# Optimization experiments

Hardware: AMD Instinct MI355X
Metric: run time of the kernel (lower is better)

The kernel has to match this reference:

```python
import jax, jax.numpy as jnp
import numpy as np

MU = 23.359
STD = 1.41
Q_LIM = 500.0
DAY = 24.0 * 3600.0
WEEK = 7.0 * DAY


def setup_inputs() -> dict:
    key = jax.random.key(0)
    ks = jax.random.split(key, 6)
    n, n_rooms, h, T, n_tout = 256, 254, 64, 50000, 2048
    m = 1 + n_rooms  # u = [Tout, Q_per_room]
    t_eval = jnp.arange(T, dtype=jnp.float32) * 30.0
    # Hurwitz A: slow RC thermal dynamics (eigenvalues ~ -1e-4 1/s)
    A = 1e-4 * (0.3 * jax.random.normal(ks[0], (n, n), jnp.float32) / np.sqrt(n)
                - jnp.eye(n, dtype=jnp.float32))
    B = 1e-6 * jax.random.uniform(ks[1], (n, m), jnp.float32)
    cooling = jax.random.uniform(ks[2], (n_rooms, 1), jnp.float32)
    w1 = 0.05 * jax.random.normal(ks[3], (h, n + 4), jnp.float32)
    b1 = jnp.zeros((h,), jnp.float32)
    w2 = 0.1 * jax.random.normal(ks[4], (h,), jnp.float32)
    # outside-temperature interpolation table covering [0, T*30+30]
    tout_ts = jnp.linspace(0.0, float(T) * 30.0 + 30.0, n_tout, dtype=jnp.float32)
    tout_vals = 10.0 + 5.0 * jax.random.normal(ks[5], (n_tout,), jnp.float32)
    return dict(t_eval=t_eval, A=A, B=B, cooling=cooling, w1=w1, b1=b1, w2=w2,
                tout_ts=tout_ts, tout_vals=tout_vals)


def _integrate(t_eval, A, B, cooling, w1, b1, w2, tout_ts, tout_vals):
    n = A.shape[0]
    # transform=sigmoid then heat_scaling(Q_lim)
    heat = jax.nn.sigmoid(cooling[:, 0]) * Q_LIM  # [n_rooms]
    t0 = t_eval[0]
    ts = t_eval - t0
    dt = ts[1] - ts[0]
    iv = 26.0 * jnp.ones((n,), jnp.float32)

    def action_of(x, t):
        xn = (x - MU) / STD
        sig = jnp.stack([jnp.sin(t * (2.0 * jnp.pi / DAY)),
                         jnp.cos(t * (2.0 * jnp.pi / DAY)),
                         jnp.sin(t * (2.0 * jnp.pi / WEEK)),
                         jnp.cos(t * (2.0 * jnp.pi / WEEK))])
        s = jnp.concatenate([xn, sig])  # [n+4]
        return jax.nn.sigmoid(jnp.dot(w2, jnp.tanh(w1 @ s + b1)))  # scalar action

    def f(x, t, Q):
        # dy/dt = A x + B u,  u = [Tout(t+t0), Q]
        Tout = jnp.interp(t + t0, tout_ts, tout_vals)
        u = jnp.concatenate([Tout[None], Q])
        return A @ x + B @ u

    def step(x, t):
        # policy action held over the RK4 substeps (30 s policy hold == dt)
        Q = -heat * action_of(x, t)
        k1 = f(x, t, Q)
        k2 = f(x + 0.5 * dt * k1, t + 0.5 * dt, Q)
        k3 = f(x + 0.5 * dt * k2, t + 0.5 * dt, Q)
        k4 = f(x + dt * k3, t + dt, Q)
        x_new = x + (dt / 6.0) * (k1 + 2.0 * k2 + 2.0 * k3 + k4)
        return x_new, x  # emit state AT t (odeint returns iv first)

    _, traj = jax.lax.scan(step, iv, ts)
    return traj  # [T, n]


_integrate_jit = jax.jit(_integrate)


def reference(t_eval, A, B, cooling, w1, b1, w2, tout_ts, tout_vals):
    return _integrate_jit(t_eval, A, B, cooling, w1, b1, w2, tout_ts, tout_vals)
```

## Files before the change

### kernel.cpp

```cpp
#include <hip/hip_runtime.h>
#include <math.h>

#define NN 256
#define HH 64

typedef unsigned int uint32;
typedef _Float16 h2f __attribute__((ext_vector_type(2)));

__device__ __forceinline__ float sigm(float x) { return 1.0f / (1.0f + expf(-x)); }

__device__ __forceinline__ float dot2(uint32 a, uint32 b, float c) {
#if __has_builtin(__builtin_amdgcn_fdot2)
    return __builtin_amdgcn_fdot2(__builtin_bit_cast(h2f, a),
                                  __builtin_bit_cast(h2f, b), c, false);
#else
    h2f x = __builtin_bit_cast(h2f, a), y = __builtin_bit_cast(h2f, b);
    return c + (float)x[0] * (float)y[0] + (float)x[1] * (float)y[1];
#endif
}

__global__ void k_affine(const float* __restrict__ A, float* __restrict__ Pout,
                         const float* __restrict__ tev, int div)
{
    int i = blockIdx.x, j = threadIdx.x;
    double h = (double)tev[1] - (double)tev[0];
    double v = (i == j ? 1.0 : 0.0) + (h / (double)div) * (double)A[i * NN + j];
    Pout[i * NN + j] = (float)v;
}

__global__ void k_gemm(const float* __restrict__ A, const float* __restrict__ Pin,
                       float* __restrict__ Pout, const float* __restrict__ tev, int div)
{
    int i = blockIdx.x, j = threadIdx.x;
    double h = (double)tev[1] - (double)tev[0];
    const float* Ar = A + i * NN;
    double acc = 0.0;
    for (int k = 0; k < NN; ++k) acc += (double)Ar[k] * (double)Pin[k * NN + j];
    double v = (i == j ? 1.0 : 0.0) + (h / (double)div) * acc;
    Pout[i * NN + j] = (float)v;
}

__global__ void k_prep_vec(const float* __restrict__ A, const float* __restrict__ B,
                           const float* __restrict__ cooling, const float* __restrict__ tev,
                           const float* __restrict__ R, float* __restrict__ gq)
{
    __shared__ float heat[NN];
    __shared__ float vin[NN];
    int t = threadIdx.x;
    double h = (double)tev[1] - (double)tev[0];
    heat[t] = (t < NN - 2) ? 500.0f * sigm(cooling[t]) : 0.0f;
    __syncthreads();
    float B0 = B[t * (NN - 1)];
    double bh = 0.0;
    for (int j = 0; j < NN - 2; ++j) bh += (double)B[t * (NN - 1) + 1 + j] * (double)heat[j];
    vin[t] = B0; __syncthreads();
    double v1 = 0.0; for (int k = 0; k < NN; ++k) v1 += (double)A[t * NN + k] * (double)vin[k];
    __syncthreads(); vin[t] = (float)v1; __syncthreads();
    double v2 = 0.0; for (int k = 0; k < NN; ++k) v2 += (double)A[t * NN + k] * (double)vin[k];
    __syncthreads(); vin[t] = (float)v2; __syncthreads();
    double v3 = 0.0; for (int k = 0; k < NN; ++k) v3 += (double)A[t * NN + k] * (double)vin[k];
    __syncthreads();
    vin[t] = (float)bh; __syncthreads();
    double u1 = 0.0; for (int k = 0; k < NN; ++k) u1 += (double)A[t * NN + k] * (double)vin[k];
    __syncthreads(); vin[t] = (float)u1; __syncthreads();
    double u2 = 0.0; for (int k = 0; k < NN; ++k) u2 += (double)A[t * NN + k] * (double)vin[k];
    __syncthreads(); vin[t] = (float)u2; __syncthreads();
    double u3 = 0.0; for (int k = 0; k < NN; ++k) u3 += (double)A[t * NN + k] * (double)vin[k];

    double srow = 0.0;
    for (int c = 0; c < NN; ++c) srow += (double)R[t * NN + c];
    srow -= 1.0;

    gq[t]        = (float)((h / 6.0) * (double)B0);
    gq[256 + t]  = (float)((h * h / 6.0) * v1);
    gq[512 + t]  = (float)((h * h * h / 12.0) * v2);
    gq[768 + t]  = (float)((h * h * h * h / 24.0) * v3);
    gq[1024 + t] = (float)(h * bh + (h * h / 2.0) * u1 + (h * h * h / 6.0) * u2
                           + (h * h * h * h / 24.0) * u3);
    gq[1280 + t] = (float)(23.359 * srow);
}

__device__ __forceinline__ float interp1(float x, const float* __restrict__ ts,
                                         const float* __restrict__ vs, int n)
{
    int lo = 0, hi = n;
    while (lo < hi) { int mid = (lo + hi) >> 1; if (ts[mid] <= x) lo = mid + 1; else hi = mid; }
    int i = lo; if (i < 1) i = 1; if (i > n - 1) i = n - 1;
    float xim = ts[i - 1], xi = ts[i];
    float fim = vs[i - 1], fi = vs[i];
    return fim + (x - xim) / (xi - xim) * (fi - fim);
}

__global__ void k_time(const float* __restrict__ tev, const float* __restrict__ tts,
                       const float* __restrict__ tvals, float* __restrict__ td,
                       int T, int ntout)
{
    int k = blockIdx.x * blockDim.x + threadIdx.x;
    if (k >= T) return;
    float t0 = tev[0];
    float dtf = tev[1] - t0;
    float t = tev[k] - t0;
    const float cD = (float)(2.0 * M_PI / 86400.0);
    const float cW = (float)(2.0 * M_PI / 604800.0);
    float f0 = (float)sin((double)(t * cD));
    float f1 = (float)cos((double)(t * cD));
    float f2 = (float)sin((double)(t * cW));
    float f3 = (float)cos((double)(t * cW));
    float To1 = interp1(t + t0, tts, tvals, ntout);
    float To2 = interp1((t + 0.5f * dtf) + t0, tts, tvals, ntout);
    float To4 = interp1((t + dtf) + t0, tts, tvals, ntout);
    size_t o = (size_t)k * 8;
    td[o + 0] = To1 + 4.0f * To2 + To4;
    td[o + 1] = To1 + 2.0f * To2;
    td[o + 2] = To1 + To2;
    td[o + 3] = To1;
    td[o + 4] = f0; td[o + 5] = f1; td[o + 6] = f2; td[o + 7] = f3;
}

__global__ void k_packE(const float* __restrict__ R, uint32* __restrict__ Epk)
{
    int d = blockIdx.x * 256 + threadIdx.x;
    int t = d >> 6, i = d & 63;
    int r = t & 255, hf = t >> 8;
    int c = hf * 128 + 2 * i;
    float e0 = 64.0f * (R[r * NN + c]     - (r == c     ? 1.0f : 0.0f));
    float e1 = 64.0f * (R[r * NN + c + 1] - (r == c + 1 ? 1.0f : 0.0f));
    union { _Float16 h[2]; uint32 u; } p;
    p.h[0] = (_Float16)e0; p.h[1] = (_Float16)e1;
    Epk[d] = p.u;
}

__global__ void k_packW(const float* __restrict__ w1, uint32* __restrict__ w1pk)
{
    int d = blockIdx.x * 256 + threadIdx.x;
    int t = d >> 4, sd = d & 15;
    int jr = t >> 3, c = t & 7;
    int j = sd >> 1, p = sd & 1;
    int col = c * 4 + j * 32 + 2 * p;
    const float is = 1.0f / 1.41f;
    union { _Float16 h[2]; uint32 u; } q;
    q.h[0] = (_Float16)(w1[jr * 260 + col] * is);
    q.h[1] = (_Float16)(w1[jr * 260 + col + 1] * is);
    w1pk[d] = q.u;
}

__global__ __launch_bounds__(512, 2) void k_main(
    const float* __restrict__ tdata, const uint32* Epk,
    const uint32* __restrict__ w1pk, const float* __restrict__ gq,
    const float* __restrict__ w1g, const float* __restrict__ b1g,
    const float* __restrict__ w2g, float* out, int T)
{
    __shared__ __align__(16) uint32 spk[132];
    __shared__ __align__(16) float xbuf[NN];
    __shared__ __align__(16) float part[2][NN];
    __shared__ float gql[6 * NN];
    __shared__ float wf[6 * HH];
    __shared__ float hid[HH];
    __shared__ float b1eff[HH];
    __shared__ float td[2][8];

    const int t = threadIdx.x;
    const int r = t & 255;
    const int hf = t >> 8;
    const int jr = t >> 3;
    const int c2 = (t & 7) * 2;
    const int lane = t & 63;

    uint32 Ereg[64];
    {
        const uint4* Eg = reinterpret_cast<const uint4*>(Epk) + (size_t)t * 16;
        #pragma unroll
        for (int i = 0; i < 16; ++i) {
            uint4 v = Eg[i];
            Ereg[4 * i + 0] = v.x; Ereg[4 * i + 1] = v.y;
            Ereg[4 * i + 2] = v.z; Ereg[4 * i + 3] = v.w;
        }
    }
    uint32 w1reg[16];
    {
        const uint4* Wg = reinterpret_cast<const uint4*>(w1pk) + (size_t)t * 4;
        #pragma unroll
        for (int i = 0; i < 4; ++i) {
            uint4 v = Wg[i];
            w1reg[4 * i + 0] = v.x; w1reg[4 * i + 1] = v.y;
            w1reg[4 * i + 2] = v.z; w1reg[4 * i + 3] = v.w;
        }
    }
    for (int i = t; i < 6 * NN; i += 512) gql[i] = gq[i];
    if (t < HH) {
        wf[t]       = w1g[t * 260 + 256];
        wf[64 + t]  = w1g[t * 260 + 257];
        wf[128 + t] = w1g[t * 260 + 258];
        wf[192 + t] = w1g[t * 260 + 259];
        wf[256 + t] = b1g[t];
        wf[320 + t] = w2g[t];
    }
    _Float16* sph = reinterpret_cast<_Float16*>(spk);
    if (t < NN) {
        xbuf[t] = 26.0f;
        sph[t] = (_Float16)(26.0f - 23.359f);
    }
    if (t < 8) td[0][t] = tdata[t];
    __syncthreads();
    if (t < HH)
        b1eff[t] = wf[256 + t] + wf[t] * td[0][4] + wf[64 + t] * td[0][5]
                 + wf[128 + t] * td[0][6] + wf[192 + t] * td[0][7];
    __syncthreads();

    const uint4* sp4 = reinterpret_cast<const uint4*>(spk);

    for (int k = 0; k < T; ++k) {
        const int cur = k & 1, nxt = cur ^ 1;
        float tdp = 0.0f;
        if (t >= 504 && k + 1 < T) tdp = tdata[(size_t)(k + 1) * 8 + (t - 504)];

        float hs = 0.0f;
        {
            #pragma unroll
            for (int j = 0; j < 8; ++j) {
                uint2 sx = *reinterpret_cast<const uint2*>(spk + c2 + j * 16);
                hs = dot2(w1reg[2 * j], sx.x, hs);
                hs = dot2(w1reg[2 * j + 1], sx.y, hs);
            }
        }
        hs += __shfl_xor(hs, 1); hs += __shfl_xor(hs, 2); hs += __shfl_xor(hs, 4);
        if ((t & 7) == 0) hid[jr] = tanhf(hs + b1eff[jr]);

        float ac0 = 0.f, ac1 = 0.f, ac2 = 0.f, ac3 = 0.f;
        const uint4* xp = sp4 + hf * 16;
        #define ECHUNK(B) { \
            uint4 q0 = xp[(B) + 0], q1 = xp[(B) + 1], q2 = xp[(B) + 2], q3 = xp[(B) + 3]; \
            ac0 = dot2(Ereg[4*(B)+ 0], q0.x, ac0); ac1 = dot2(Ereg[4*(B)+ 1], q0.y, ac1); \
            ac2 = dot2(Ereg[4*(B)+ 2], q0.z, ac2); ac3 = dot2(Ereg[4*(B)+ 3], q0.w, ac3); \
            ac0 = dot2(Ereg[4*(B)+ 4], q1.x, ac0); ac1 = dot2(Ereg[4*(B)+ 5], q1.y, ac1); \
            ac2 = dot2(Ereg[4*(B)+ 6], q1.z, ac2); ac3 = dot2(Ereg[4*(B)+ 7], q1.w, ac3); \
            ac0 = dot2(Ereg[4*(B)+ 8], q2.x, ac0); ac1 = dot2(Ereg[4*(B)+ 9], q2.y, ac1); \
            ac2 = dot2(Ereg[4*(B)+10], q2.z, ac2); ac3 = dot2(Ereg[4*(B)+11], q2.w, ac3); \
            ac0 = dot2(Ereg[4*(B)+12], q3.x, ac0); ac1 = dot2(Ereg[4*(B)+13], q3.y, ac1); \
            ac2 = dot2(Ereg[4*(B)+14], q3.z, ac2); ac3 = dot2(Ereg[4*(B)+15], q3.w, ac3); }
        ECHUNK(0)
        __builtin_amdgcn_sched_barrier(0);
        ECHUNK(4)
        __builtin_amdgcn_sched_barrier(0);
        ECHUNK(8)
        __builtin_amdgcn_sched_barrier(0);
        ECHUNK(12)
        #undef ECHUNK
        part[hf][r] = (ac0 + ac1) + (ac2 + ac3);

        if (t < NN) out[(size_t)k * NN + t] = xbuf[t];
        if (t >= 504) td[nxt][t - 504] = tdp;
        asm volatile("s_waitcnt lgkmcnt(0)\ns_barrier" ::: "memory");

        if (t < NN) {
            float v = wf[320 + lane] * hid[lane];
            v += __shfl_xor(v, 1);  v += __shfl_xor(v, 2);  v += __shfl_xor(v, 4);
            v += __shfl_xor(v, 8);  v += __shfl_xor(v, 16); v += __shfl_xor(v, 32);
            float aS = sigm(v);
            float S0 = td[cur][0], S1 = td[cur][1], S2 = td[cur][2], S3 = td[cur][3];
            float y = (part[0][t] + part[1][t]) * 0.015625f;
            float xn = xbuf[t] + y + gql[1280 + t]
                     + S0 * gql[t] + S1 * gql[256 + t] + S2 * gql[512 + t]
                     + S3 * gql[768 + t] - aS * gql[1024 + t];
            xbuf[t] = xn;
            sph[t] = (_Float16)(xn - 23.359f);
        } else if (t < 320 && k + 1 < T) {
            int j = t - 256;
            b1eff[j] = wf[256 + j] + wf[j] * td[nxt][4] + wf[64 + j] * td[nxt][5]
                     + wf[128 + j] * td[nxt][6] + wf[192 + j] * td[nxt][7];
        }
        asm volatile("s_waitcnt lgkmcnt(0)\ns_barrier" ::: "memory");
    }
}

extern "C" void kernel_launch(void* const* d_in, const int* in_sizes, int n_in,
                              void* d_out, int out_size, void* d_ws, size_t ws_size,
                              hipStream_t stream)
{
    (void)n_in; (void)out_size; (void)ws_size;
    const float* tev     = (const float*)d_in[0];
    const float* A       = (const float*)d_in[1];
    const float* B       = (const float*)d_in[2];
    const float* cooling = (const float*)d_in[3];
    const float* w1      = (const float*)d_in[4];
    const float* b1      = (const float*)d_in[5];
    const float* w2      = (const float*)d_in[6];
    const float* tts     = (const float*)d_in[7];
    const float* tvals   = (const float*)d_in[8];
    const int T     = in_sizes[0];
    const int ntout = in_sizes[7];

    float* out = (float*)d_out;
    float* ws  = (float*)d_ws;
    float*  R    = ws;
    float*  gq   = ws + 65536;
    uint32* w1pk = (uint32*)(ws + 67072);
    float*  td   = ws + 75264;
    float* P1 = out;
    float* P2 = out + 65536;
    size_t outN = (size_t)T * NN;
    uint32* Epk = (uint32*)(out + outN - 32768);

    hipLaunchKernelGGL(k_affine, dim3(256), dim3(256), 0, stream, A, P1, tev, 4);
    hipLaunchKernelGGL(k_gemm,   dim3(256), dim3(256), 0, stream, A, P1, P2, tev, 3);
    hipLaunchKernelGGL(k_gemm,   dim3(256), dim3(256), 0, stream, A, P2, P1, tev, 2);
    hipLaunchKernelGGL(k_gemm,   dim3(256), dim3(256), 0, stream, A, P1, R,  tev, 1);
    hipLaunchKernelGGL(k_packE,  dim3(128), dim3(256), 0, stream, R, Epk);
    hipLaunchKernelGGL(k_packW,  dim3(32),  dim3(256), 0, stream, w1, w1pk);
    hipLaunchKernelGGL(k_prep_vec, dim3(1), dim3(256), 0, stream, A, B, cooling, tev, R, gq);
    hipLaunchKernelGGL(k_time, dim3((T + 255) / 256), dim3(256), 0, stream,
                       tev, tts, tvals, td, T, ntout);
    hipLaunchKernelGGL(k_main, dim3(1), dim3(512), 0, stream,
                       td, Epk, w1pk, gq, w1, b1, w2, out, T);
}
```

Measured before the change: 60.56 ms.

## Use one thread per state row with full-row register-resident propagator

```diff
diff --git a/kernel.cpp b/kernel.cpp
--- a/kernel.cpp
+++ b/kernel.cpp
@@ -9,7 +9,7 @@
 
 __device__ __forceinline__ float sigm(float x) { return 1.0f / (1.0f + expf(-x)); }
 
-__device__ __forceinline__ float dot2(uint32 a, uint32 b, float c) {
+__device__ __forceinline__ float dot2f(float a, uint32 b, float c) {
 #if __has_builtin(__builtin_amdgcn_fdot2)
     return __builtin_amdgcn_fdot2(__builtin_bit_cast(h2f, a),
                                   __builtin_bit_cast(h2f, b), c, false);
@@ -120,9 +120,8 @@
 __global__ void k_packE(const float* __restrict__ R, uint32* __restrict__ Epk)
 {
     int d = blockIdx.x * 256 + threadIdx.x;
-    int t = d >> 6, i = d & 63;
-    int r = t & 255, hf = t >> 8;
-    int c = hf * 128 + 2 * i;
+    int r = d >> 7, i = d & 127;
+    int c = 2 * i;
     float e0 = 64.0f * (R[r * NN + c]     - (r == c     ? 1.0f : 0.0f));
     float e1 = 64.0f * (R[r * NN + c + 1] - (r == c + 1 ? 1.0f : 0.0f));
     union { _Float16 h[2]; uint32 u; } p;
@@ -133,60 +132,50 @@
 __global__ void k_packW(const float* __restrict__ w1, uint32* __restrict__ w1pk)
 {
     int d = blockIdx.x * 256 + threadIdx.x;
-    int t = d >> 4, sd = d & 15;
-    int jr = t >> 3, c = t & 7;
-    int j = sd >> 1, p = sd & 1;
-    int col = c * 4 + j * 32 + 2 * p;
+    int t = d >> 5, s = d & 31;
+    int jr = t >> 2, c = t & 3;
+    int j = s >> 2, q = s & 3;
+    int col = 2 * (16 * j + 4 * c + q);
     const float is = 1.0f / 1.41f;
-    union { _Float16 h[2]; uint32 u; } q;
-    q.h[0] = (_Float16)(w1[jr * 260 + col] * is);
-    q.h[1] = (_Float16)(w1[jr * 260 + col + 1] * is);
-    w1pk[d] = q.u;
-}
-
-__global__ __launch_bounds__(512, 2) void k_main(
-    const float* __restrict__ tdata, const uint32* Epk,
-    const uint32* __restrict__ w1pk, const float* __restrict__ gq,
-    const float* __restrict__ w1g, const float* __restrict__ b1g,
-    const float* __restrict__ w2g, float* out, int T)
+    union { _Float16 h[2]; uint32 u; } p;
+    p.h[0] = (_Float16)(w1[jr * 260 + col] * is);
+    p.h[1] = (_Float16)(w1[jr * 260 + col + 1] * is);
+    w1pk[d] = p.u;
+}
+
+__global__ __launch_bounds__(256, 1) void k_main(
+    const float* __restrict__ tdata, const float* Epk, const float* w1pk,
+    const float* gq, const float* __restrict__ w1g,
+    const float* __restrict__ b1g, const float* __restrict__ w2g,
+    float* out, int T)
 {
     __shared__ __align__(16) uint32 spk[132];
-    __shared__ __align__(16) float xbuf[NN];
-    __shared__ __align__(16) float part[2][NN];
-    __shared__ float gql[6 * NN];
     __shared__ float wf[6 * HH];
     __shared__ float hid[HH];
     __shared__ float b1eff[HH];
     __shared__ float td[2][8];
 
     const int t = threadIdx.x;
-    const int r = t & 255;
-    const int hf = t >> 8;
-    const int jr = t >> 3;
-    const int c2 = (t & 7) * 2;
+    const int jr = t >> 2;
+    const int c = t & 3;
     const int lane = t & 63;
 
-    uint32 Ereg[64];
+    float4 Ereg[32];
     {
-        const uint4* Eg = reinterpret_cast<const uint4*>(Epk) + (size_t)t * 16;
+        const float4* Eg = reinterpret_cast<const float4*>(Epk) + (size_t)t * 32;
         #pragma unroll
-        for (int i = 0; i < 16; ++i) {
-            uint4 v = Eg[i];
-            Ereg[4 * i + 0] = v.x; Ereg[4 * i + 1] = v.y;
-            Ereg[4 * i + 2] = v.z; Ereg[4 * i + 3] = v.w;
-        }
-    }
-    uint32 w1reg[16];
+        for (int i = 0; i < 32; ++i) Ereg[i] = Eg[i];
+    }
+    float4 Wreg[8];
     {
-        const uint4* Wg = reinterpret_cast<const uint4*>(w1pk) + (size_t)t * 4;
+        const float4* Wg = reinterpret_cast<const float4*>(w1pk) + (size_t)t * 8;
         #pragma unroll
-        for (int i = 0; i < 4; ++i) {
-            uint4 v = Wg[i];
-            w1reg[4 * i + 0] = v.x; w1reg[4 * i + 1] = v.y;
-            w1reg[4 * i + 2] = v.z; w1reg[4 * i + 3] = v.w;
-        }
-    }
-    for (int i = t; i < 6 * NN; i += 512) gql[i] = gq[i];
+        for (int i = 0; i < 8; ++i) Wreg[i] = Wg[i];
+    }
+    float g0r = gq[t], g1r = gq[256 + t], g2r = gq[512 + t], g3r = gq[768 + t];
+    float qr = gq[1024 + t], cer = gq[1280 + t];
+    float w2r = w2g[lane];
+
     if (t < HH) {
         wf[t]       = w1g[t * 260 + 256];
         wf[64 + t]  = w1g[t * 260 + 257];
@@ -196,10 +185,8 @@
         wf[320 + t] = w2g[t];
     }
     _Float16* sph = reinterpret_cast<_Float16*>(spk);
-    if (t < NN) {
-        xbuf[t] = 26.0f;
-        sph[t] = (_Float16)(26.0f - 23.359f);
-    }
+    float xr = 26.0f;
+    sph[t] = (_Float16)(26.0f - 23.359f);
     if (t < 8) td[0][t] = tdata[t];
     __syncthreads();
     if (t < HH)
@@ -212,63 +199,53 @@
     for (int k = 0; k < T; ++k) {
         const int cur = k & 1, nxt = cur ^ 1;
         float tdp = 0.0f;
-        if (t >= 504 && k + 1 < T) tdp = tdata[(size_t)(k + 1) * 8 + (t - 504)];
+        if (t >= 248 && k + 1 < T) tdp = tdata[(size_t)(k + 1) * 8 + (t - 248)];
 
         float hs = 0.0f;
         {
             #pragma unroll
             for (int j = 0; j < 8; ++j) {
-                uint2 sx = *reinterpret_cast<const uint2*>(spk + c2 + j * 16);
-                hs = dot2(w1reg[2 * j], sx.x, hs);
-                hs = dot2(w1reg[2 * j + 1], sx.y, hs);
+                uint4 sx = sp4[4 * j + c];
+                float4 w = Wreg[j];
+                hs = dot2f(w.x, sx.x, hs); hs = dot2f(w.y, sx.y, hs);
+                hs = dot2f(w.z, sx.z, hs); hs = dot2f(w.w, sx.w, hs);
             }
         }
-        hs += __shfl_xor(hs, 1); hs += __shfl_xor(hs, 2); hs += __shfl_xor(hs, 4);
-        if ((t & 7) == 0) hid[jr] = tanhf(hs + b1eff[jr]);
+        hs += __shfl_xor(hs, 1); hs += __shfl_xor(hs, 2);
+        if (c == 0) hid[jr] = tanhf(hs + b1eff[jr]);
 
         float ac0 = 0.f, ac1 = 0.f, ac2 = 0.f, ac3 = 0.f;
-        const uint4* xp = sp4 + hf * 16;
-        #define ECHUNK(B) { \
-            uint4 q0 = xp[(B) + 0], q1 = xp[(B) + 1], q2 = xp[(B) + 2], q3 = xp[(B) + 3]; \
-            ac0 = dot2(Ereg[4*(B)+ 0], q0.x, ac0); ac1 = dot2(Ereg[4*(B)+ 1], q0.y, ac1); \
-            ac2 = dot2(Ereg[4*(B)+ 2], q0.z, ac2); ac3 = dot2(Ereg[4*(B)+ 3], q0.w, ac3); \
-            ac0 = dot2(Ereg[4*(B)+ 4], q1.x, ac0); ac1 = dot2(Ereg[4*(B)+ 5], q1.y, ac1); \
-            ac2 = dot2(Ereg[4*(B)+ 6], q1.z, ac2); ac3 = dot2(Ereg[4*(B)+ 7], q1.w, ac3); \
-            ac0 = dot2(Ereg[4*(B)+ 8], q2.x, ac0); ac1 = dot2(Ereg[4*(B)+ 9], q2.y, ac1); \
-            ac2 = dot2(Ereg[4*(B)+10], q2.z, ac2); ac3 = dot2(Ereg[4*(B)+11], q2.w, ac3); \
-            ac0 = dot2(Ereg[4*(B)+12], q3.x, ac0); ac1 = dot2(Ereg[4*(B)+13], q3.y, ac1); \
-            ac2 = dot2(Ereg[4*(B)+14], q3.z, ac2); ac3 = dot2(Ereg[4*(B)+15], q3.w, ac3); }
-        ECHUNK(0)
-        __builtin_amdgcn_sched_barrier(0);
-        ECHUNK(4)
-        __builtin_amdgcn_sched_barrier(0);
-        ECHUNK(8)
-        __builtin_amdgcn_sched_barrier(0);
-        ECHUNK(12)
-        #undef ECHUNK
-        part[hf][r] = (ac0 + ac1) + (ac2 + ac3);
-
-        if (t < NN) out[(size_t)k * NN + t] = xbuf[t];
-        if (t >= 504) td[nxt][t - 504] = tdp;
+        {
+            #pragma unroll
+            for (int i = 0; i < 32; ++i) {
+                uint4 xq = sp4[i];
+                float4 e = Ereg[i];
+                ac0 = dot2f(e.x, xq.x, ac0);
+                ac1 = dot2f(e.y, xq.y, ac1);
+                ac2 = dot2f(e.z, xq.z, ac2);
+                ac3 = dot2f(e.w, xq.w, ac3);
+            }
+        }
+        float y = (ac0 + ac1) + (ac2 + ac3);
+
+        out[(size_t)k * NN + t] = xr;
+        if (t >= 248) td[nxt][t - 248] = tdp;
         asm volatile("s_waitcnt lgkmcnt(0)\ns_barrier" ::: "memory");
 
-        if (t < NN) {
-            float v = wf[320 + lane] * hid[lane];
+        {
+            float v = w2r * hid[lane];
             v += __shfl_xor(v, 1);  v += __shfl_xor(v, 2);  v += __shfl_xor(v, 4);
             v += __shfl_xor(v, 8);  v += __shfl_xor(v, 16); v += __shfl_xor(v, 32);
             float aS = sigm(v);
             float S0 = td[cur][0], S1 = td[cur][1], S2 = td[cur][2], S3 = td[cur][3];
-            float y = (part[0][t] + part[1][t]) * 0.015625f;
-            float xn = xbuf[t] + y + gql[1280 + t]
-                     + S0 * gql[t] + S1 * gql[256 + t] + S2 * gql[512 + t]
-                     + S3 * gql[768 + t] - aS * gql[1024 + t];
-            xbuf[t] = xn;
+            float xn = xr + y * 0.015625f + cer
+                     + S0 * g0r + S1 * g1r + S2 * g2r + S3 * g3r - aS * qr;
+            xr = xn;
             sph[t] = (_Float16)(xn - 23.359f);
-        } else if (t < 320 && k + 1 < T) {
-            int j = t - 256;
-            b1eff[j] = wf[256 + j] + wf[j] * td[nxt][4] + wf[64 + j] * td[nxt][5]
-                     + wf[128 + j] * td[nxt][6] + wf[192 + j] * td[nxt][7];
         }
+        if (t < HH && k + 1 < T)
+            b1eff[t] = wf[256 + t] + wf[t] * td[nxt][4] + wf[64 + t] * td[nxt][5]
+                     + wf[128 + t] * td[nxt][6] + wf[192 + t] * td[nxt][7];
         asm volatile("s_waitcnt lgkmcnt(0)\ns_barrier" ::: "memory");
     }
 }
@@ -310,6 +287,6 @@
     hipLaunchKernelGGL(k_prep_vec, dim3(1), dim3(256), 0, stream, A, B, cooling, tev, R, gq);
     hipLaunchKernelGGL(k_time, dim3((T + 255) / 256), dim3(256), 0, stream,
                        tev, tts, tvals, td, T, ntout);
-    hipLaunchKernelGGL(k_main, dim3(1), dim3(512), 0, stream,
-                       td, Epk, w1pk, gq, w1, b1, w2, out, T);
-}
+    hipLaunchKernelGGL(k_main, dim3(1), dim3(256), 0, stream,
+                       td, (const float*)Epk, (const float*)w1pk, gq, w1, b1, w2, out, T);
+}
```

Result: slower. 69.42 ms (+14.6%).
